# Optimization experiments

Hardware: AMD Instinct MI355X
Metric: run time of the kernel (lower is better)

## Reference

```python
import jax, jax.numpy as jnp
import numpy as np

TEMPERATURE = 0.07
BN_EPS = 1e-5
NORM_EPS = 1e-12


def _forward_features(x, conv_w, conv_b, gamma, beta, lin_w, lin_b):
    # prepend_relu
    x = jax.nn.relu(x)
    # 1x1 conv: [B, Cin, H, W] x [Cout, Cin] -> [B, Cout, H, W]
    x = jnp.einsum('bihw,oi->bohw', x, conv_w) + conv_b[None, :, None, None]
    # BatchNorm2d, training mode (biased batch stats over N,H,W per channel)
    mu = x.mean(axis=(0, 2, 3))
    var = x.var(axis=(0, 2, 3))
    x = (x - mu[None, :, None, None]) * jax.lax.rsqrt(var + BN_EPS)[None, :, None, None]
    x = x * gamma[None, :, None, None] + beta[None, :, None, None]
    x = jax.nn.relu(x)
    # second 1x1 conv ('linear')
    x = jnp.einsum('bihw,oi->bohw', x, lin_w) + lin_b[None, :, None, None]
    # append_normalize: F.normalize(p=2, dim=1)
    norm = jnp.sqrt(jnp.sum(x * x, axis=1, keepdims=True))
    x = x / jnp.maximum(norm, NORM_EPS)
    return x


def _dense_info_nce(o, t):
    # o, t: [B, C, H, W]
    B, C, H, W = t.shape
    o = o.transpose(0, 2, 3, 1).reshape(B, H * W, C)  # [B, HW, C]
    t = t.transpose(0, 2, 3, 1).reshape(B, H * W, C)
    pos = jnp.einsum('bik,bik->bi', o, t) / TEMPERATURE          # [B, HW]
    logits = jnp.einsum('bik,bjk->bij', o, t) / TEMPERATURE      # [B, HW, HW]
    lse = jax.nn.logsumexp(logits, axis=-1)                      # [B, HW]
    return jnp.mean(lse - pos)


def setup_inputs() -> dict:
    key = jax.random.key(0)
    ks = jax.random.split(key, 4)
    B, Cin, Cout, H, W = 8, 256, 128, 60, 60
    x_orig = jax.random.normal(ks[0], (B, Cin, H, W), jnp.float32)
    x_trans = jax.random.normal(ks[1], (B, Cin, H, W), jnp.float32)
    conv_w = jax.random.normal(ks[2], (Cout, Cin), jnp.float32) * (1.0 / np.sqrt(Cin))
    conv_b = jnp.zeros((Cout,), jnp.float32)
    gamma = jnp.ones((Cout,), jnp.float32)
    beta = jnp.zeros((Cout,), jnp.float32)
    lin_w = jax.random.normal(ks[3], (Cout, Cout), jnp.float32) * (1.0 / np.sqrt(Cout))
    lin_b = jnp.zeros((Cout,), jnp.float32)
    return {"x_orig": x_orig, "x_trans": x_trans, "conv_w": conv_w, "conv_b": conv_b,
            "gamma": gamma, "beta": beta, "lin_w": lin_w, "lin_b": lin_b}


def reference(x_orig, x_trans, conv_w, conv_b, gamma, beta, lin_w, lin_b):
    o = _forward_features(x_orig, conv_w, conv_b, gamma, beta, lin_w, lin_b)
    t = _forward_features(x_trans, conv_w, conv_b, gamma, beta, lin_w, lin_b)
    return _dense_info_nce(o, t)
```

## Files before the change

### kernel.cpp

```cpp
#include <hip/hip_runtime.h>
#include <hip/hip_bf16.h>

#define HW 3600
#define NQ 28800
#define CIN 256
#define CMID 128
#define NSHARD 16

typedef short bf16x8 __attribute__((ext_vector_type(8)));
typedef float f32x4 __attribute__((ext_vector_type(4)));

#define INV_T 14.285714285714286f
#define SQRT_INV_T 3.7796447300922722f
#define LOG2E 1.4426950408889634f
#define NM (-20.60992915555662f)

__device__ inline unsigned short f2bf(float f) {
  unsigned u = __float_as_uint(f);
  return (unsigned short)((u + 0x7fffu + ((u >> 16) & 1u)) >> 16);
}
__device__ inline float bf2f(unsigned short h) { return __uint_as_float((unsigned)h << 16); }

__global__ void prep_kernel(const float* __restrict__ conv_w, const float* __restrict__ lin_w,
                            unsigned short* __restrict__ cw16, unsigned short* __restrict__ lw16) {
  const int i = blockIdx.x * 256 + threadIdx.x;
  if (i < 128 * 256) cw16[i] = f2bf(conv_w[i]);
  if (i < 128 * 128) lw16[i] = f2bf(lin_w[i]);
}

__global__ __launch_bounds__(256, 4) void conv1_mfma_kernel(
    const float* __restrict__ x0, const float* __restrict__ x1,
    const unsigned short* __restrict__ cw16,
    unsigned short* __restrict__ yt, float* __restrict__ stats) {
  __shared__ __align__(16) unsigned short xT[64 * 32];
  __shared__ float sredw[4][128];
  __shared__ float s2redw[4][128];
  const int z = blockIdx.z;
  const float* x = z ? x1 : x0;
  float* st = stats + (z * NSHARD + (blockIdx.x & (NSHARD - 1))) * 256;
  unsigned short* yz = yt + (size_t)z * NQ * 128;

  const int t = threadIdx.x;
  const int w = t >> 6;
  const int l = t & 63;
  const int lr = l & 15;
  const int lg = l >> 4;
  const int q0 = blockIdx.x * 64;

  f32x4 acc[8];
#pragma unroll
  for (int tile = 0; tile < 8; tile++) acc[tile] = (f32x4){0.f, 0.f, 0.f, 0.f};

  const int qcol = q0 + 4 * (t & 15);
  const int bb = qcol / HW;
  const int pp = qcol - bb * HW;
  const float* xcol = x + (size_t)bb * CIN * HW + pp;
  const int cil0 = (t >> 4);
  const int cil1 = cil0 + 16;

  float4 v0 = *(const float4*)&xcol[(size_t)cil0 * HW];
  float4 v1 = *(const float4*)&xcol[(size_t)cil1 * HW];

  for (int ch = 0; ch < 8; ch++) {
    if (ch) __syncthreads();
    {
      unsigned short* dst = &xT[(4 * (t & 15)) * 32 + cil0];
      dst[0]  = f2bf(fmaxf(v0.x, 0.f));
      dst[32] = f2bf(fmaxf(v0.y, 0.f));
      dst[64] = f2bf(fmaxf(v0.z, 0.f));
      dst[96] = f2bf(fmaxf(v0.w, 0.f));
      dst = &xT[(4 * (t & 15)) * 32 + cil1];
      dst[0]  = f2bf(fmaxf(v1.x, 0.f));
      dst[32] = f2bf(fmaxf(v1.y, 0.f));
      dst[64] = f2bf(fmaxf(v1.z, 0.f));
      dst[96] = f2bf(fmaxf(v1.w, 0.f));
    }
    __syncthreads();
    if (ch < 7) {
      v0 = *(const float4*)&xcol[(size_t)((ch + 1) * 32 + cil0) * HW];
      v1 = *(const float4*)&xcol[(size_t)((ch + 1) * 32 + cil1) * HW];
    }
    bf16x8 bv = *(const bf16x8*)&xT[(w * 16 + lr) * 32 + lg * 8];
#pragma unroll
    for (int tile = 0; tile < 8; tile++) {
      bf16x8 av = *(const bf16x8*)&cw16[(size_t)(tile * 16 + lr) * 256 + ch * 32 + lg * 8];
      acc[tile] = __builtin_amdgcn_mfma_f32_16x16x32_bf16(av, bv, acc[tile], 0, 0, 0);
    }
  }

#pragma unroll
  for (int tile = 0; tile < 8; tile++) {
#pragma unroll
    for (int i = 0; i < 4; i++) {
      float v = acc[tile][i];
      float v2 = v * v;
      v += __shfl_xor(v, 1); v2 += __shfl_xor(v2, 1);
      v += __shfl_xor(v, 2); v2 += __shfl_xor(v2, 2);
      v += __shfl_xor(v, 4); v2 += __shfl_xor(v2, 4);
      v += __shfl_xor(v, 8); v2 += __shfl_xor(v2, 8);
      if (lr == 0) {
        sredw[w][tile * 16 + lg * 4 + i] = v;
        s2redw[w][tile * 16 + lg * 4 + i] = v2;
      }
    }
  }

  const int q = q0 + w * 16 + lr;
#pragma unroll
  for (int tile = 0; tile < 8; tile++) {
    union { unsigned short u[4]; uint2 v; } pk;
#pragma unroll
    for (int i = 0; i < 4; i++) pk.u[i] = f2bf(acc[tile][i]);
    *(uint2*)&yz[(size_t)q * 128 + tile * 16 + lg * 4] = pk.v;
  }

  __syncthreads();
  if (t < 128) {
    atomicAdd(&st[t], sredw[0][t] + sredw[1][t] + sredw[2][t] + sredw[3][t]);
    atomicAdd(&st[128 + t], s2redw[0][t] + s2redw[1][t] + s2redw[2][t] + s2redw[3][t]);
  }
}

__global__ void scale_kernel(const float* __restrict__ stats, const float* __restrict__ conv_b,
                             const float* __restrict__ gamma, const float* __restrict__ beta,
                             float* __restrict__ sc) {
  const int z = blockIdx.x;
  const float* st = stats + z * NSHARD * 256;
  float* scz = sc + z * 256;
  const int c = threadIdx.x;
  float s1 = 0.f, s2 = 0.f;
#pragma unroll
  for (int sh = 0; sh < NSHARD; sh++) {
    s1 += st[sh * 256 + c];
    s2 += st[sh * 256 + 128 + c];
  }
  const float inv_n = 1.f / (float)NQ;
  const float macc = s1 * inv_n;
  const float var = s2 * inv_n - macc * macc;
  const float mean = macc + conv_b[c];
  const float s = gamma[c] * rsqrtf(var + 1e-5f);
  const float tt = beta[c] - mean * s;
  scz[c] = s;
  scz[128 + c] = conv_b[c] * s + tt;
}

__global__ __launch_bounds__(256, 4) void conv2_mfma_kernel(
    const unsigned short* __restrict__ yt, const unsigned short* __restrict__ lw16,
    const float* __restrict__ sc, const float* __restrict__ lin_b,
    unsigned short* __restrict__ feat_o, unsigned short* __restrict__ feat_t) {
  const int z = blockIdx.z;
  const unsigned short* yz = yt + (size_t)z * NQ * 128;
  const float* scz = sc + z * 256;
  unsigned short* feat = z ? feat_t : feat_o;

  const int t = threadIdx.x;
  const int w = t >> 6;
  const int l = t & 63;
  const int lr = l & 15;
  const int lg = l >> 4;
  const int q = blockIdx.x * 64 + w * 16 + lr;

  f32x4 acc[8];
#pragma unroll
  for (int tile = 0; tile < 8; tile++) acc[tile] = (f32x4){0.f, 0.f, 0.f, 0.f};

  const unsigned short* yrow = yz + (size_t)q * 128;
  for (int ch = 0; ch < 4; ch++) {
    bf16x8 raw = *(const bf16x8*)&yrow[ch * 32 + lg * 8];
    bf16x8 bv;
#pragma unroll
    for (int e = 0; e < 8; e++) {
      const int c = ch * 32 + lg * 8 + e;
      float v = fmaxf(fmaf(bf2f((unsigned short)raw[e]), scz[c], scz[128 + c]), 0.f);
      bv[e] = (short)f2bf(v);
    }
#pragma unroll
    for (int tile = 0; tile < 8; tile++) {
      bf16x8 av = *(const bf16x8*)&lw16[(size_t)(tile * 16 + lr) * 128 + ch * 32 + lg * 8];
      acc[tile] = __builtin_amdgcn_mfma_f32_16x16x32_bf16(av, bv, acc[tile], 0, 0, 0);
    }
  }

  float vals[8][4];
  float ssq = 0.f;
#pragma unroll
  for (int tile = 0; tile < 8; tile++) {
#pragma unroll
    for (int i = 0; i < 4; i++) {
      float v = acc[tile][i] + lin_b[tile * 16 + lg * 4 + i];
      vals[tile][i] = v;
      ssq += v * v;
    }
  }
  ssq += __shfl_xor(ssq, 16);
  ssq += __shfl_xor(ssq, 32);
  const float inv = SQRT_INV_T / fmaxf(sqrtf(ssq), 1e-12f);

#pragma unroll
  for (int tile = 0; tile < 8; tile++) {
    union { unsigned short u[4]; uint2 v; } pk;
#pragma unroll
    for (int i = 0; i < 4; i++) pk.u[i] = f2bf(vals[tile][i] * inv);
    *(uint2*)&feat[(size_t)q * 128 + tile * 16 + tile * 0 + lg * 4] = pk.v;
  }
}

__global__ __launch_bounds__(256, 2) void infonce_kernel(
    const unsigned short* __restrict__ fo, const unsigned short* __restrict__ ft,
    float* __restrict__ sumexp) {
  __shared__ __align__(16) unsigned short Bs[2][6144];
  const int id = blockIdx.x;
  const int b = id & 7;
  const int within = id >> 3;
  const int rowblk = within % 15;
  const int colg = within / 15;
  const int t = threadIdx.x;
  const int w = t >> 6;
  const int lane = t & 63;
  const int lr = lane & 15;
  const int lkq = lane >> 4;
  const int base = rowblk * 256 + w * 64;
  const unsigned short* fob = fo + (size_t)b * HW * 128;
  const unsigned short* ftb = ft + (size_t)b * HW * 128;

  bf16x8 a[4][4];
#pragma unroll
  for (int tile = 0; tile < 4; tile++) {
    const int r = min(base + tile * 16 + lr, HW - 1);
    const unsigned short* ap = fob + (size_t)r * 128 + lkq * 8;
#pragma unroll
    for (int kk = 0; kk < 4; kk++) a[tile][kk] = *(const bf16x8*)(ap + kk * 32);
  }
  float rs[4][4];
#pragma unroll
  for (int tile = 0; tile < 4; tile++)
#pragma unroll
    for (int i = 0; i < 4; i++) rs[tile][i] = 0.f;

  int rowoff[3];
#pragma unroll
  for (int i = 0; i < 3; i++) {
    const int f = i * 4 + w;
    const int kk = f / 3;
    const int sub = f - kk * 3;
    rowoff[i] = (sub * 16 + lr) * 128 + kk * 32 + lkq * 8;
  }

  uint4 r[3];
  {
    const unsigned short* p = ftb + (size_t)(colg * 15) * 48 * 128;
#pragma unroll
    for (int i = 0; i < 3; i++) r[i] = *(const uint4*)(p + rowoff[i]);
  }

  for (int it = 0; it < 15; it++) {
    unsigned short* bufp = &Bs[it & 1][0];
#pragma unroll
    for (int i = 0; i < 3; i++)
      *(uint4*)&bufp[(i * 4 + w) * 512 + lane * 8] = r[i];
    __syncthreads();
    if (it < 14) {
      const unsigned short* p = ftb + (size_t)((colg * 15 + it + 1)) * 48 * 128;
#pragma unroll
      for (int i = 0; i < 3; i++) r[i] = *(const uint4*)(p + rowoff[i]);
    }
    f32x4 acc[4][3];
#pragma unroll
    for (int tile = 0; tile < 4; tile++)
#pragma unroll
      for (int sub = 0; sub < 3; sub++) acc[tile][sub] = (f32x4){0.f, 0.f, 0.f, 0.f};
#pragma unroll
    for (int kk = 0; kk < 4; kk++) {
      bf16x8 bv[3];
#pragma unroll
      for (int sub = 0; sub < 3; sub++)
        bv[sub] = *(const bf16x8*)&bufp[(kk * 3 + sub) * 512 + lane * 8];
#pragma unroll
      for (int tile = 0; tile < 4; tile++)
#pragma unroll
        for (int sub = 0; sub < 3; sub++)
          acc[tile][sub] = __builtin_amdgcn_mfma_f32_16x16x32_bf16(
              a[tile][kk], bv[sub], acc[tile][sub], 0, 0, 0);
    }
#pragma unroll
    for (int tile = 0; tile < 4; tile++)
#pragma unroll
      for (int sub = 0; sub < 3; sub++)
#pragma unroll
        for (int i = 0; i < 4; i++)
          rs[tile][i] += exp2f(fmaf(acc[tile][sub][i], LOG2E, NM));
  }

#pragma unroll
  for (int tile = 0; tile < 4; tile++)
#pragma unroll
    for (int i = 0; i < 4; i++) {
      float v = rs[tile][i];
      v += __shfl_xor(v, 1); v += __shfl_xor(v, 2);
      v += __shfl_xor(v, 4); v += __shfl_xor(v, 8);
      rs[tile][i] = v;
    }
  if (lr == 0) {
#pragma unroll
    for (int tile = 0; tile < 4; tile++)
#pragma unroll
      for (int i = 0; i < 4; i++) {
        const int rr = base + tile * 16 + lkq * 4 + i;
        if (rr < HW) atomicAdd(&sumexp[b * HW + rr], rs[tile][i]);
      }
  }
}

__global__ __launch_bounds__(256) void final_kernel(
    const float* __restrict__ sumexp, const unsigned short* __restrict__ fo,
    const unsigned short* __restrict__ ft, float* __restrict__ out) {
  const int q = blockIdx.x * 256 + threadIdx.x;
  float val = 0.f;
  if (q < NQ) {
    const unsigned short* a = fo + (size_t)q * 128;
    const unsigned short* c = ft + (size_t)q * 128;
    float dot = 0.f;
#pragma unroll
    for (int k = 0; k < 128; k += 8) {
      bf16x8 ua = *(const bf16x8*)(a + k);
      bf16x8 ub = *(const bf16x8*)(c + k);
#pragma unroll
      for (int e = 0; e < 8; e++)
        dot = fmaf(bf2f((unsigned short)ua[e]), bf2f((unsigned short)ub[e]), dot);
    }
    val = logf(sumexp[q]) + INV_T - dot;
  }
#pragma unroll
  for (int m = 1; m < 64; m <<= 1) val += __shfl_xor(val, m);
  __shared__ float red[4];
  const int wid = threadIdx.x >> 6;
  if ((threadIdx.x & 63) == 0) red[wid] = val;
  __syncthreads();
  if (threadIdx.x == 0)
    atomicAdd(out, (red[0] + red[1] + red[2] + red[3]) * (1.f / (float)NQ));
}

extern "C" void kernel_launch(void* const* d_in, const int* in_sizes, int n_in,
                              void* d_out, int out_size, void* d_ws, size_t ws_size,
                              hipStream_t stream) {
  (void)in_sizes; (void)n_in; (void)out_size; (void)ws_size;
  const float* x_orig = (const float*)d_in[0];
  const float* x_trans = (const float*)d_in[1];
  const float* conv_w = (const float*)d_in[2];
  const float* conv_b = (const float*)d_in[3];
  const float* gamma = (const float*)d_in[4];
  const float* beta = (const float*)d_in[5];
  const float* lin_w = (const float*)d_in[6];
  const float* lin_b = (const float*)d_in[7];
  float* out = (float*)d_out;

  char* ws = (char*)d_ws;
  unsigned short* yt = (unsigned short*)(ws + 0);
  unsigned short* cw16 = (unsigned short*)(ws + 14745600);
  unsigned short* lw16 = (unsigned short*)(ws + 14811136);
  float* stats = (float*)(ws + 14843904);
  float* sc = (float*)(ws + 14876672);
  float* sumexp = (float*)(ws + 14878720);
  unsigned short* feat_o = (unsigned short*)(ws + 14993920);
  unsigned short* feat_t = (unsigned short*)(ws + 22366720);

  hipMemsetAsync(ws + 14843904, 0, 32768 + 2048 + 115200, stream);
  hipMemsetAsync(d_out, 0, sizeof(float), stream);

  prep_kernel<<<128, 256, 0, stream>>>(conv_w, lin_w, cw16, lw16);

  conv1_mfma_kernel<<<dim3(450, 1, 2), 256, 0, stream>>>(x_orig, x_trans, cw16, yt, stats);
  scale_kernel<<<2, 128, 0, stream>>>(stats, conv_b, gamma, beta, sc);
  conv2_mfma_kernel<<<dim3(450, 1, 2), 256, 0, stream>>>(yt, lw16, sc, lin_b, feat_o, feat_t);

  infonce_kernel<<<600, 256, 0, stream>>>(feat_o, feat_t, sumexp);
  final_kernel<<<113, 256, 0, stream>>>(sumexp, feat_o, feat_t, out);
}
```

Baseline: 250.1 us.

## Split InfoNCE columns finer, drop atomics and max shift, swizzle conv1 LDS

The InfoNCE kernel now runs 1800 blocks, each covering 5 column tiles instead of 15, with launch bounds raised to 4 blocks per CU. Each block writes its partial row sums to a per-column-group slab, and the final kernel adds up the 15 slabs, so the atomics and the sumexp memset are gone. The normalization scale now folds log2(e)/T into the features, so exp2 takes the raw MFMA output and the fixed max-shift FMA disappears. Without that shift, exp2 of values up to about 20.6 stays well within float range. Conv1 pads and XOR-swizzles its LDS transpose tile to avoid bank conflicts. The slab reuses the yt workspace region, which is only safe because conv2 has already finished with yt.

```diff
diff --git a/kernel.cpp b/kernel.cpp
--- a/kernel.cpp
+++ b/kernel.cpp
@@ -11,9 +11,8 @@
 typedef float f32x4 __attribute__((ext_vector_type(4)));
 
 #define INV_T 14.285714285714286f
-#define SQRT_INV_T 3.7796447300922722f
-#define LOG2E 1.4426950408889634f
-#define NM (-20.60992915555662f)
+#define SQRT_SCALE 4.539816f
+#define LN2F 0.6931471805599453f
 
 __device__ inline unsigned short f2bf(float f) {
   unsigned u = __float_as_uint(f);
@@ -32,7 +31,7 @@
     const float* __restrict__ x0, const float* __restrict__ x1,
     const unsigned short* __restrict__ cw16,
     unsigned short* __restrict__ yt, float* __restrict__ stats) {
-  __shared__ __align__(16) unsigned short xT[64 * 32];
+  __shared__ __align__(16) unsigned short xT[64 * 40];
   __shared__ float sredw[4][128];
   __shared__ float s2redw[4][128];
   const int z = blockIdx.z;
@@ -51,36 +50,41 @@
 #pragma unroll
   for (int tile = 0; tile < 8; tile++) acc[tile] = (f32x4){0.f, 0.f, 0.f, 0.f};
 
-  const int qcol = q0 + 4 * (t & 15);
+  const int kq = t & 15;
+  const int qcol = q0 + 4 * kq;
   const int bb = qcol / HW;
   const int pp = qcol - bb * HW;
   const float* xcol = x + (size_t)bb * CIN * HW + pp;
   const int cil0 = (t >> 4);
   const int cil1 = cil0 + 16;
+  const int c0s = (cil0 & 7) | ((((cil0 >> 3) ^ kq) & 3) << 3);
+  const int c1s = (cil1 & 7) | ((((cil1 >> 3) ^ kq) & 3) << 3);
 
   float4 v0 = *(const float4*)&xcol[(size_t)cil0 * HW];
   float4 v1 = *(const float4*)&xcol[(size_t)cil1 * HW];
+
+  const int rdoff = (w * 16 + lr) * 40 + (((lg ^ ((w * 16 + lr) >> 2)) & 3) << 3);
 
   for (int ch = 0; ch < 8; ch++) {
     if (ch) __syncthreads();
     {
-      unsigned short* dst = &xT[(4 * (t & 15)) * 32 + cil0];
-      dst[0]  = f2bf(fmaxf(v0.x, 0.f));
-      dst[32] = f2bf(fmaxf(v0.y, 0.f));
-      dst[64] = f2bf(fmaxf(v0.z, 0.f));
-      dst[96] = f2bf(fmaxf(v0.w, 0.f));
-      dst = &xT[(4 * (t & 15)) * 32 + cil1];
-      dst[0]  = f2bf(fmaxf(v1.x, 0.f));
-      dst[32] = f2bf(fmaxf(v1.y, 0.f));
-      dst[64] = f2bf(fmaxf(v1.z, 0.f));
-      dst[96] = f2bf(fmaxf(v1.w, 0.f));
+      unsigned short* dst = &xT[(4 * kq) * 40 + c0s];
+      dst[0]   = f2bf(fmaxf(v0.x, 0.f));
+      dst[40]  = f2bf(fmaxf(v0.y, 0.f));
+      dst[80]  = f2bf(fmaxf(v0.z, 0.f));
+      dst[120] = f2bf(fmaxf(v0.w, 0.f));
+      dst = &xT[(4 * kq) * 40 + c1s];
+      dst[0]   = f2bf(fmaxf(v1.x, 0.f));
+      dst[40]  = f2bf(fmaxf(v1.y, 0.f));
+      dst[80]  = f2bf(fmaxf(v1.z, 0.f));
+      dst[120] = f2bf(fmaxf(v1.w, 0.f));
     }
     __syncthreads();
     if (ch < 7) {
       v0 = *(const float4*)&xcol[(size_t)((ch + 1) * 32 + cil0) * HW];
       v1 = *(const float4*)&xcol[(size_t)((ch + 1) * 32 + cil1) * HW];
     }
-    bf16x8 bv = *(const bf16x8*)&xT[(w * 16 + lr) * 32 + lg * 8];
+    bf16x8 bv = *(const bf16x8*)&xT[rdoff];
 #pragma unroll
     for (int tile = 0; tile < 8; tile++) {
       bf16x8 av = *(const bf16x8*)&cw16[(size_t)(tile * 16 + lr) * 256 + ch * 32 + lg * 8];
@@ -194,20 +198,20 @@
   }
   ssq += __shfl_xor(ssq, 16);
   ssq += __shfl_xor(ssq, 32);
-  const float inv = SQRT_INV_T / fmaxf(sqrtf(ssq), 1e-12f);
+  const float inv = SQRT_SCALE / fmaxf(sqrtf(ssq), 1e-12f);
 
 #pragma unroll
   for (int tile = 0; tile < 8; tile++) {
     union { unsigned short u[4]; uint2 v; } pk;
 #pragma unroll
     for (int i = 0; i < 4; i++) pk.u[i] = f2bf(vals[tile][i] * inv);
-    *(uint2*)&feat[(size_t)q * 128 + tile * 16 + tile * 0 + lg * 4] = pk.v;
-  }
-}
-
-__global__ __launch_bounds__(256, 2) void infonce_kernel(
+    *(uint2*)&feat[(size_t)q * 128 + tile * 16 + lg * 4] = pk.v;
+  }
+}
+
+__global__ __launch_bounds__(256, 4) void infonce_kernel(
     const unsigned short* __restrict__ fo, const unsigned short* __restrict__ ft,
-    float* __restrict__ sumexp) {
+    float* __restrict__ slab) {
   __shared__ __align__(16) unsigned short Bs[2][6144];
   const int id = blockIdx.x;
   const int b = id & 7;
@@ -248,19 +252,19 @@
 
   uint4 r[3];
   {
-    const unsigned short* p = ftb + (size_t)(colg * 15) * 48 * 128;
+    const unsigned short* p = ftb + (size_t)(colg * 5) * 48 * 128;
 #pragma unroll
     for (int i = 0; i < 3; i++) r[i] = *(const uint4*)(p + rowoff[i]);
   }
 
-  for (int it = 0; it < 15; it++) {
+  for (int it = 0; it < 5; it++) {
     unsigned short* bufp = &Bs[it & 1][0];
 #pragma unroll
     for (int i = 0; i < 3; i++)
       *(uint4*)&bufp[(i * 4 + w) * 512 + lane * 8] = r[i];
     __syncthreads();
-    if (it < 14) {
-      const unsigned short* p = ftb + (size_t)((colg * 15 + it + 1)) * 48 * 128;
+    if (it < 4) {
+      const unsigned short* p = ftb + (size_t)(colg * 5 + it + 1) * 48 * 128;
 #pragma unroll
       for (int i = 0; i < 3; i++) r[i] = *(const uint4*)(p + rowoff[i]);
     }
@@ -288,7 +292,7 @@
       for (int sub = 0; sub < 3; sub++)
 #pragma unroll
         for (int i = 0; i < 4; i++)
-          rs[tile][i] += exp2f(fmaf(acc[tile][sub][i], LOG2E, NM));
+          rs[tile][i] += exp2f(acc[tile][sub][i]);
   }
 
 #pragma unroll
@@ -301,22 +305,26 @@
       rs[tile][i] = v;
     }
   if (lr == 0) {
+    float* out = slab + (size_t)colg * NQ + b * HW;
 #pragma unroll
     for (int tile = 0; tile < 4; tile++)
 #pragma unroll
       for (int i = 0; i < 4; i++) {
         const int rr = base + tile * 16 + lkq * 4 + i;
-        if (rr < HW) atomicAdd(&sumexp[b * HW + rr], rs[tile][i]);
+        if (rr < HW) out[rr] = rs[tile][i];
       }
   }
 }
 
 __global__ __launch_bounds__(256) void final_kernel(
-    const float* __restrict__ sumexp, const unsigned short* __restrict__ fo,
+    const float* __restrict__ slab, const unsigned short* __restrict__ fo,
     const unsigned short* __restrict__ ft, float* __restrict__ out) {
   const int q = blockIdx.x * 256 + threadIdx.x;
   float val = 0.f;
   if (q < NQ) {
+    float se = 0.f;
+#pragma unroll
+    for (int s = 0; s < 15; s++) se += slab[(size_t)s * NQ + q];
     const unsigned short* a = fo + (size_t)q * 128;
     const unsigned short* c = ft + (size_t)q * 128;
     float dot = 0.f;
@@ -328,7 +336,7 @@
       for (int e = 0; e < 8; e++)
         dot = fmaf(bf2f((unsigned short)ua[e]), bf2f((unsigned short)ub[e]), dot);
     }
-    val = logf(sumexp[q]) + INV_T - dot;
+    val = logf(se) - dot * LN2F;
   }
 #pragma unroll
   for (int m = 1; m < 64; m <<= 1) val += __shfl_xor(val, m);
@@ -356,15 +364,15 @@
 
   char* ws = (char*)d_ws;
   unsigned short* yt = (unsigned short*)(ws + 0);
+  float* slab = (float*)(ws + 0);
   unsigned short* cw16 = (unsigned short*)(ws + 14745600);
   unsigned short* lw16 = (unsigned short*)(ws + 14811136);
   float* stats = (float*)(ws + 14843904);
   float* sc = (float*)(ws + 14876672);
-  float* sumexp = (float*)(ws + 14878720);
-  unsigned short* feat_o = (unsigned short*)(ws + 14993920);
-  unsigned short* feat_t = (unsigned short*)(ws + 22366720);
-
-  hipMemsetAsync(ws + 14843904, 0, 32768 + 2048 + 115200, stream);
+  unsigned short* feat_o = (unsigned short*)(ws + 14878720);
+  unsigned short* feat_t = (unsigned short*)(ws + 22251520);
+
+  hipMemsetAsync(stats, 0, 32768, stream);
   hipMemsetAsync(d_out, 0, sizeof(float), stream);
 
   prep_kernel<<<128, 256, 0, stream>>>(conv_w, lin_w, cw16, lw16);
@@ -373,6 +381,6 @@
   scale_kernel<<<2, 128, 0, stream>>>(stats, conv_b, gamma, beta, sc);
   conv2_mfma_kernel<<<dim3(450, 1, 2), 256, 0, stream>>>(yt, lw16, sc, lin_b, feat_o, feat_t);
 
-  infonce_kernel<<<600, 256, 0, stream>>>(feat_o, feat_t, sumexp);
-  final_kernel<<<113, 256, 0, stream>>>(sumexp, feat_o, feat_t, out);
-}
+  infonce_kernel<<<1800, 256, 0, stream>>>(feat_o, feat_t, slab);
+  final_kernel<<<113, 256, 0, stream>>>(slab, feat_o, feat_t, out);
+}
```

Measured after the change: 300.6 us. 1.2x slower.
